# Optimization experiments

Measured on AMD Instinct MI355X. Metric: run time of the kernel, lower is better.

## Reference

```python
import jax, jax.numpy as jnp
import numpy as np

D = 32      # d_shape (internal width, also propagate_dimensions and out_channels)
S = 3       # space_dimensions
K = 40      # kNN neighbors
EPS = 1e-5  # BatchNorm1d eps


def _elu(x):
    return jax.nn.elu(x)


def _batchnorm(x, gamma, beta):
    # training-mode BatchNorm1d over all nodes (flattened batch*nodes), biased var
    mu = x.mean(axis=(0, 1))
    var = x.var(axis=(0, 1))
    return gamma * (x - mu) / jnp.sqrt(var + EPS) + beta


def _knn_mean_max(s, h):
    # s: [N, S] learned coords, h: [N, D] propagated features (one graph)
    N = s.shape[0]
    n2 = jnp.sum(s * s, axis=-1)                     # [N]
    d2 = n2[:, None] + n2[None, :] - 2.0 * (s @ s.T)  # [N, N] squared dists
    d2 = jnp.maximum(d2, 0.0)
    d2 = jnp.where(jnp.eye(N, dtype=bool), jnp.inf, d2)  # exclude self loops
    _, idx = jax.lax.top_k(-d2, K)                   # idx: [N, K] neighbor (src) ids per dst
    d2_sel = jnp.take_along_axis(d2, idx, axis=1)    # [N, K]
    pot = jnp.exp(-d2_sel)                           # gaussian potential exp(-||ds||^2)
    msg = pot[..., None] * h[idx]                    # [N, K, D] edge messages
    return jnp.concatenate([msg.mean(axis=1), msg.max(axis=1)], axis=-1)  # [N, 2D]


def setup_inputs() -> dict:
    key = jax.random.key(0)
    ks = jax.random.split(key, 12)
    B, N, C = 2, 8192, 9

    def lin_w(k, i, o):
        return (jax.random.normal(k, (i, o), jnp.float32) / np.sqrt(i)).astype(jnp.float32)

    return {
        "x": jax.random.normal(ks[0], (B, N, C), jnp.float32),
        # pre_gravnet: Linear(C->32), ELU, Linear(32->32), ELU
        "pre_W1": lin_w(ks[1], C, D), "pre_b1": jnp.zeros((D,), jnp.float32),
        "pre_W2": lin_w(ks[2], D, D), "pre_b2": jnp.zeros((D,), jnp.float32),
        "bn1_g": jnp.ones((D,), jnp.float32), "bn1_b": jnp.zeros((D,), jnp.float32),
        # GravNetConv: lin_s (no bias), lin_h, lin (in = D + 2D -> D)
        "lin_s_W": lin_w(ks[3], D, S),
        "lin_h_W": lin_w(ks[4], D, D), "lin_h_b": jnp.zeros((D,), jnp.float32),
        "lin_W": lin_w(ks[5], D + 2 * D, D), "lin_b": jnp.zeros((D,), jnp.float32),
        # post_gravnet: Linear(D+S+D -> 32), ELU, Linear(32->32), ELU
        "post_W1": lin_w(ks[6], D + S + D, D), "post_b1": jnp.zeros((D,), jnp.float32),
        "post_W2": lin_w(ks[7], D, D), "post_b2": jnp.zeros((D,), jnp.float32),
        "bn2_g": jnp.ones((D,), jnp.float32), "bn2_b": jnp.zeros((D,), jnp.float32),
    }


def reference(x, pre_W1, pre_b1, pre_W2, pre_b2, bn1_g, bn1_b,
              lin_s_W, lin_h_W, lin_h_b, lin_W, lin_b,
              post_W1, post_b1, post_W2, post_b2, bn2_g, bn2_b):
    # pre_gravnet MLP + batchnorm
    x1 = _elu(_elu(x @ pre_W1 + pre_b1) @ pre_W2 + pre_b2)
    x1 = _batchnorm(x1, bn1_g, bn1_b)

    # GravNetConv
    h_l = x1 @ lin_h_W + lin_h_b     # [B, N, D]
    s_l = x1 @ lin_s_W               # [B, N, S] learned coords
    agg = jax.vmap(_knn_mean_max)(s_l, h_l)           # [B, N, 2D]
    xgn = jnp.concatenate([agg, x1], axis=-1) @ lin_W + lin_b  # [B, N, D]

    # post_gravnet MLP + batchnorm
    xc = jnp.concatenate([xgn, s_l, x1], axis=-1)     # [B, N, D+S+D]
    out = _elu(_elu(xc @ post_W1 + post_b1) @ post_W2 + post_b2)
    out = _batchnorm(out, bn2_g, bn2_b)
    return out
```

## Files before the change

### kernel.cpp

```cpp
#include <hip/hip_runtime.h>
#include <math.h>

#define NN    8192
#define NODES 16384
#define KK    40
#define CAP   256


__device__ __forceinline__ float r15_elu(float x){ return x > 0.f ? x : expm1f(x); }

__device__ __forceinline__ unsigned r15_key(float4 si, float4 sj){
  float dot = si.x*sj.x + si.y*sj.y + si.z*sj.z;
  float d2 = si.w + sj.w - 2.0f*dot;
  d2 = fmaxf(d2, 0.0f);
  return __float_as_uint(d2);
}

__global__ __launch_bounds__(256) void r15_pre(const float* __restrict__ x,
    const float* __restrict__ W1, const float* __restrict__ b1,
    const float* __restrict__ W2, const float* __restrict__ b2,
    float* __restrict__ xpre, float* __restrict__ part1)
{
  __shared__ float sW1[9*32], sb1[32], sW2[32*32], sb2[32];
  __shared__ float wls[4][32], wls2[4][32];
  int t = threadIdx.x;
  for (int i = t; i < 9*32;  i += 256) sW1[i] = W1[i];
  for (int i = t; i < 32*32; i += 256) sW2[i] = W2[i];
  if (t < 32) { sb1[t] = b1[t]; sb2[t] = b2[t]; }
  __syncthreads();
  int node = blockIdx.x*256 + t;
  float xv[9], a1[32], a2[32];
  #pragma unroll
  for (int i=0;i<9;i++) xv[i] = x[node*9+i];
  #pragma unroll
  for (int o=0;o<32;o++){
    float a = sb1[o];
    #pragma unroll
    for (int i=0;i<9;i++) a += xv[i]*sW1[i*32+o];
    a1[o] = r15_elu(a);
  }
  #pragma unroll
  for (int o=0;o<32;o++){
    float a = sb2[o];
    #pragma unroll
    for (int i=0;i<32;i++) a += a1[i]*sW2[i*32+o];
    a2[o] = r15_elu(a);
    xpre[(size_t)node*32+o] = a2[o];
  }
  int lane = t & 63, w = t >> 6;
  #pragma unroll
  for (int c=0;c<32;c++){
    float v = a2[c], v2 = a2[c]*a2[c];
    #pragma unroll
    for (int off=32; off; off>>=1){ v += __shfl_down(v,(unsigned)off,64); v2 += __shfl_down(v2,(unsigned)off,64); }
    if (lane==0){ wls[w][c]=v; wls2[w][c]=v2; }
  }
  __syncthreads();
  if (t < 32){
    part1[blockIdx.x*64 + t]      = wls[0][t]+wls[1][t]+wls[2][t]+wls[3][t];
    part1[blockIdx.x*64 + 32 + t] = wls2[0][t]+wls2[1][t]+wls2[2][t]+wls2[3][t];
  }
}

__global__ __launch_bounds__(256) void r15_bnproj(const float* __restrict__ part1,
    const float* __restrict__ xpre,
    const float* __restrict__ bng, const float* __restrict__ bnb,
    const float* __restrict__ hW, const float* __restrict__ hb, const float* __restrict__ sW,
    float* __restrict__ x1, float* __restrict__ h, float4* __restrict__ s4)
{
  __shared__ float sHW[32*32], sHB[32], sSW[32*3];
  __shared__ float sstat[64];
  __shared__ float smu[32], sdev[32], sg[32], sbt[32];
  int t = threadIdx.x;
  for (int i=t;i<1024;i+=256) sHW[i]=hW[i];
  if (t < 96) sSW[t]=sW[t];
  if (t < 64){
    float s = 0.f;
    for (int b2=0;b2<64;b2++) s += part1[b2*64+t];
    sstat[t] = s;
  }
  __syncthreads();
  if (t < 32){
    sHB[t]=hb[t];
    float s = sstat[t], sq = sstat[32+t];
    float mu = s * (1.f/NODES);
    float var = sq * (1.f/NODES) - mu*mu;
    smu[t]=mu; sdev[t]=sqrtf(var+1e-5f);
    sg[t]=bng[t]; sbt[t]=bnb[t];
  }
  __syncthreads();
  int node = blockIdx.x*256+t;
  float v[32];
  #pragma unroll
  for (int c=0;c<32;c++){
    float a = xpre[(size_t)node*32+c];
    v[c] = sg[c]*(a - smu[c])/sdev[c] + sbt[c];
    x1[(size_t)node*32+c] = v[c];
  }
  #pragma unroll
  for (int o=0;o<32;o++){
    float a = sHB[o];
    #pragma unroll
    for (int i=0;i<32;i++) a += v[i]*sHW[i*32+o];
    h[(size_t)node*32+o] = a;
  }
  float s0=0.f,s1=0.f,s2=0.f;
  #pragma unroll
  for (int i=0;i<32;i++){
    s0 += v[i]*sSW[i*3+0];
    s1 += v[i]*sSW[i*3+1];
    s2 += v[i]*sSW[i*3+2];
  }
  float n2 = s0*s0 + s1*s1 + s2*s2;
  s4[node] = make_float4(s0,s1,s2,n2);
}

__global__ __launch_bounds__(256) void r15_knn(const float4* __restrict__ s4,
    const float* __restrict__ h, float* __restrict__ agg)
{
  __shared__ unsigned hist[4][1024];
  __shared__ int      sel[4][KK];
  __shared__ unsigned selk[4][KK];
  __shared__ float    pots[4][KK];
  __shared__ unsigned wsum[4];
  __shared__ unsigned wtot[4][4];
  __shared__ unsigned sB1[4], sL1[4], candCount[4];

  int t = threadIdx.x;
  int lane = t & 63, w = t >> 6;
  int b  = blockIdx.x >> 11;
  int i0 = (blockIdx.x & 2047) * 4;
  const float4* sb = s4 + (size_t)b*NN;
  float4 si[4]; int iq[4];
  #pragma unroll
  for (int q=0;q<4;q++){ iq[q] = i0+q; si[q] = sb[i0+q]; }

  unsigned* histf = (unsigned*)hist;
  #pragma unroll
  for (int z=0; z<16; ++z) histf[z*256 + t] = 0u;
  if (t < 4) candCount[t] = 0u;
  __syncthreads();

  #pragma unroll 2
  for (int c=0;c<32;c++){
    int j = c*256 + t;
    float4 sj = sb[j];
    #pragma unroll
    for (int q=0;q<4;q++){
      unsigned k = r15_key(si[q], sj);
      if (j == iq[q]) k = 0x7F800000u;
      atomicAdd(&hist[q][k>>21], 1u);
    }
  }
  __syncthreads();

  for (int q=0;q<4;q++){
    unsigned c0 = hist[q][4*t+0], c1 = hist[q][4*t+1], c2 = hist[q][4*t+2], c3 = hist[q][4*t+3];
    unsigned chunk = c0+c1+c2+c3;
    unsigned sc = chunk;
    #pragma unroll
    for (int off=1; off<64; off<<=1){
      unsigned o = __shfl_up(sc, (unsigned)off, 64);
      if (lane >= off) sc += o;
    }
    if (lane == 63) wsum[w] = sc;
    __syncthreads();
    unsigned base = 0;
    for (int w2=0; w2<w; ++w2) base += wsum[w2];
    unsigned excl = base + sc - chunk;
    if (excl < KK && KK <= excl + chunk){
      unsigned acc = excl; int bb = 4*t;
      if (acc + c0 >= KK){ sB1[q] = (unsigned)bb;   sL1[q] = acc; }
      else { acc += c0;
        if (acc + c1 >= KK){ sB1[q] = (unsigned)(bb+1); sL1[q] = acc; }
        else { acc += c1;
          if (acc + c2 >= KK){ sB1[q] = (unsigned)(bb+2); sL1[q] = acc; }
          else { acc += c2;    sB1[q] = (unsigned)(bb+3); sL1[q] = acc; } } }
    }
    __syncthreads();
  }
  unsigned B1r[4];
  #pragma unroll
  for (int q=0;q<4;q++) B1r[q] = sB1[q];
  unsigned* candk = &histf[0];
  unsigned* candj = &histf[1024];

  unsigned lessm[4] = {0,0,0,0};
  unsigned cnt[4]   = {0,0,0,0};
  #pragma unroll 2
  for (int c=0;c<32;c++){
    int j = c*256 + t;
    float4 sj = sb[j];
    #pragma unroll
    for (int q=0;q<4;q++){
      unsigned k = r15_key(si[q], sj);
      if (j == iq[q]) k = 0x7F800000u;
      unsigned bin = k >> 21;
      if (bin < B1r[q]){ lessm[q] |= 1u<<c; cnt[q]++; }
      else if (bin == B1r[q]){
        unsigned slot = atomicAdd(&candCount[q], 1u);
        if (slot < CAP){ candk[q*CAP+slot] = k; candj[q*CAP+slot] = (unsigned)j; }
      }
    }
  }
  unsigned vq[4];
  #pragma unroll
  for (int q=0;q<4;q++){
    unsigned v = cnt[q];
    #pragma unroll
    for (int off=1; off<64; off<<=1){
      unsigned o = __shfl_up(v, (unsigned)off, 64);
      if (lane >= off) v += o;
    }
    if (lane == 63) wtot[q][w] = v;
    vq[q] = v;
  }
  __syncthreads();
  #pragma unroll
  for (int q=0;q<4;q++){
    unsigned gbase = 0;
    for (int w2=0; w2<w; ++w2) gbase += wtot[q][w2];
    unsigned offs = gbase + vq[q] - cnt[q];
    unsigned m = lessm[q];
    while (m){
      int c = __builtin_ctz(m); m &= m-1u;
      sel[q][offs++] = c*256 + t;
    }
  }
  __syncthreads();

  for (int q=0;q<4;q++){
    unsigned C1 = candCount[q]; if (C1 > CAP) C1 = CAP;
    unsigned L1 = sL1[q];
    for (unsigned idx = (unsigned)t; idx < C1; idx += 256){
      unsigned k = candk[q*CAP+idx], j = candj[q*CAP+idx];
      unsigned rank = L1;
      for (unsigned u=0; u<C1; ++u){
        unsigned ku = candk[q*CAP+u], ju = candj[q*CAP+u];
        rank += (ku < k || (ku == k && ju < j)) ? 1u : 0u;
      }
      if (rank < KK){ sel[q][rank] = (int)j; selk[q][rank] = k; }
    }
  }
  __syncthreads();
  #pragma unroll
  for (int q=0;q<4;q++){
    if (t < (int)sL1[q]) selk[q][t] = r15_key(si[q], sb[sel[q][t]]);
  }
  __syncthreads();
  if (t < KK){
    #pragma unroll
    for (int q=0;q<4;q++) pots[q][t] = expf(-__uint_as_float(selk[q][t]));
  }
  __syncthreads();

  float (*psum)[32] = (float(*)[32])&histf[2048];
  float (*pmax)[32] = (float(*)[32])&histf[2304];
  int ch = t & 31, g = t >> 5;
  const float* hb2 = h + (size_t)b*NN*32;
  for (int q=0;q<4;q++){
    float sum = 0.f, mx = -INFINITY;
    #pragma unroll
    for (int p=0;p<5;p++){
      int k2 = g*5 + p;
      float m = pots[q][k2] * hb2[(size_t)sel[q][k2]*32 + ch];
      sum += m; mx = fmaxf(mx, m);
    }
    psum[g][ch] = sum; pmax[g][ch] = mx;
    __syncthreads();
    if (t < 32){
      float s = 0.f, m2 = -INFINITY;
      #pragma unroll
      for (int g2=0;g2<8;g2++){ s += psum[g2][t]; m2 = fmaxf(m2, pmax[g2][t]); }
      float* ab = agg + (size_t)(b*NN + i0 + q)*64;
      ab[t]    = s / 40.0f;
      ab[32+t] = m2;
    }
    __syncthreads();
  }
}

__global__ __launch_bounds__(256) void r15_post(const float* __restrict__ agg,
    const float* __restrict__ x1, const float4* __restrict__ s4,
    const float* __restrict__ linW, const float* __restrict__ linb,
    const float* __restrict__ pW1, const float* __restrict__ pb1,
    const float* __restrict__ pW2, const float* __restrict__ pb2,
    float* __restrict__ outpre, float* __restrict__ part2)
{
  __shared__ float sLW[96*32], sPW1[67*32], sPW2[32*32];
  __shared__ float sLB[32], sPB1[32], sPB2[32];
  __shared__ float wls[4][32], wls2[4][32];
  int t = threadIdx.x;
  for (int i=t;i<96*32;i+=256) sLW[i]=linW[i];
  for (int i=t;i<67*32;i+=256) sPW1[i]=pW1[i];
  for (int i=t;i<32*32;i+=256) sPW2[i]=pW2[i];
  if (t<32){ sLB[t]=linb[t]; sPB1[t]=pb1[t]; sPB2[t]=pb2[t]; }
  __syncthreads();
  int node = blockIdx.x*256+t;
  float av[64], xv[32];
  #pragma unroll
  for (int i=0;i<64;i++) av[i]=agg[(size_t)node*64+i];
  #pragma unroll
  for (int i=0;i<32;i++) xv[i]=x1[(size_t)node*32+i];
  float4 sv = s4[node];
  float xgn[32];
  #pragma unroll
  for (int o=0;o<32;o++){
    float a = sLB[o];
    #pragma unroll
    for (int i=0;i<64;i++) a += av[i]*sLW[i*32+o];
    #pragma unroll
    for (int i=0;i<32;i++) a += xv[i]*sLW[(64+i)*32+o];
    xgn[o]=a;
  }
  float p1[32];
  #pragma unroll
  for (int o=0;o<32;o++){
    float a = sPB1[o];
    #pragma unroll
    for (int i=0;i<32;i++) a += xgn[i]*sPW1[i*32+o];
    a += sv.x*sPW1[32*32+o] + sv.y*sPW1[33*32+o] + sv.z*sPW1[34*32+o];
    #pragma unroll
    for (int i=0;i<32;i++) a += xv[i]*sPW1[(35+i)*32+o];
    p1[o]=r15_elu(a);
  }
  float p2[32];
  #pragma unroll
  for (int o=0;o<32;o++){
    float a = sPB2[o];
    #pragma unroll
    for (int i=0;i<32;i++) a += p1[i]*sPW2[i*32+o];
    p2[o] = r15_elu(a);
    outpre[(size_t)node*32+o] = p2[o];
  }
  int lane = t & 63, w = t >> 6;
  #pragma unroll
  for (int c=0;c<32;c++){
    float v = p2[c], v2 = p2[c]*p2[c];
    #pragma unroll
    for (int off=32; off; off>>=1){ v += __shfl_down(v,(unsigned)off,64); v2 += __shfl_down(v2,(unsigned)off,64); }
    if (lane==0){ wls[w][c]=v; wls2[w][c]=v2; }
  }
  __syncthreads();
  if (t < 32){
    part2[blockIdx.x*64 + t]      = wls[0][t]+wls[1][t]+wls[2][t]+wls[3][t];
    part2[blockIdx.x*64 + 32 + t] = wls2[0][t]+wls2[1][t]+wls2[2][t]+wls2[3][t];
  }
}

__global__ __launch_bounds__(256) void r15_bnout(const float* __restrict__ part2,
    const float* __restrict__ outpre,
    const float* __restrict__ g, const float* __restrict__ b,
    float* __restrict__ out)
{
  __shared__ float sstat[64];
  __shared__ float smu[32], sdev2[32], sg2[32], sb2[32];
  int t = threadIdx.x;
  if (t < 64){
    float s = 0.f;
    for (int b2=0;b2<64;b2++) s += part2[b2*64+t];
    sstat[t] = s;
  }
  __syncthreads();
  if (t < 32){
    float s = sstat[t], sq = sstat[32+t];
    float mu = s * (1.f/NODES);
    float var = sq*(1.f/NODES) - mu*mu;
    smu[t] = mu; sdev2[t] = sqrtf(var+1e-5f);
    sg2[t] = g[t]; sb2[t] = b[t];
  }
  __syncthreads();
  int idx = blockIdx.x*256 + t;
  int c = idx & 31;
  out[idx] = sg2[c]*(outpre[idx]-smu[c])/sdev2[c] + sb2[c];
}

extern "C" void kernel_launch(void* const* d_in, const int* in_sizes, int n_in,
                              void* d_out, int out_size, void* d_ws, size_t ws_size,
                              hipStream_t stream)
{
  (void)in_sizes; (void)n_in; (void)out_size; (void)ws_size;
  const float* x      = (const float*)d_in[0];
  const float* preW1  = (const float*)d_in[1];
  const float* preb1  = (const float*)d_in[2];
  const float* preW2  = (const float*)d_in[3];
  const float* preb2  = (const float*)d_in[4];
  const float* bn1g   = (const float*)d_in[5];
  const float* bn1b   = (const float*)d_in[6];
  const float* linsW  = (const float*)d_in[7];
  const float* linhW  = (const float*)d_in[8];
  const float* linhb  = (const float*)d_in[9];
  const float* linW   = (const float*)d_in[10];
  const float* linb   = (const float*)d_in[11];
  const float* postW1 = (const float*)d_in[12];
  const float* postb1 = (const float*)d_in[13];
  const float* postW2 = (const float*)d_in[14];
  const float* postb2 = (const float*)d_in[15];
  const float* bn2g   = (const float*)d_in[16];
  const float* bn2b   = (const float*)d_in[17];

  float* ws = (float*)d_ws;
  float* xpre   = ws;
  float* x1     = xpre   + (size_t)NODES*32;
  float* h      = x1     + (size_t)NODES*32;
  float* s4     = h      + (size_t)NODES*32;
  float* agg    = s4     + (size_t)NODES*4;
  float* outpre = agg    + (size_t)NODES*64;
  float* part1  = outpre + (size_t)NODES*32;
  float* part2  = part1  + 64*64;

  hipLaunchKernelGGL(r15_pre,    dim3(64),    dim3(256), 0, stream, x, preW1, preb1, preW2, preb2, xpre, part1);
  hipLaunchKernelGGL(r15_bnproj, dim3(64),    dim3(256), 0, stream, part1, xpre, bn1g, bn1b, linhW, linhb, linsW, x1, h, (float4*)s4);
  hipLaunchKernelGGL(r15_knn,    dim3(4096),  dim3(256), 0, stream, (const float4*)s4, h, agg);
  hipLaunchKernelGGL(r15_post,   dim3(64),    dim3(256), 0, stream, agg, x1, (const float4*)s4, linW, linb, postW1, postb1, postW2, postb2, outpre, part2);
  hipLaunchKernelGGL(r15_bnout,  dim3(2048),  dim3(256), 0, stream, part2, outpre, bn2g, bn2b, (float*)d_out);
}
```

Before: 233.4 us.

## Pack kNN histograms into 16-bit halves and process queries per-wave in parallel

The kNN kernel packs two queries' histograms into the low and high 16-bit halves of each shared word, halving histogram LDS from 16KB to 8KB. The threshold-bin search now runs one query per wavefront in parallel with no block-level barriers, where before it looped over queries with two syncs each. Candidate ranking and the mean/max reduction are likewise split per wave or per query, with a single barrier. This is meant to cut barrier count and LDS footprint, which may raise occupancy. The 16-bit counters are safe since each query has at most 8192 neighbours.

Measured after the change: 229.1 us. No clear change (-1.8%).

```diff
diff --git a/kernel.cpp b/kernel.cpp
--- a/kernel.cpp
+++ b/kernel.cpp
@@ -7,16 +7,16 @@
 #define CAP   256
 
 
-__device__ __forceinline__ float r15_elu(float x){ return x > 0.f ? x : expm1f(x); }
-
-__device__ __forceinline__ unsigned r15_key(float4 si, float4 sj){
+__device__ __forceinline__ float r16_elu(float x){ return x > 0.f ? x : expm1f(x); }
+
+__device__ __forceinline__ unsigned r16_key(float4 si, float4 sj){
   float dot = si.x*sj.x + si.y*sj.y + si.z*sj.z;
   float d2 = si.w + sj.w - 2.0f*dot;
   d2 = fmaxf(d2, 0.0f);
   return __float_as_uint(d2);
 }
 
-__global__ __launch_bounds__(256) void r15_pre(const float* __restrict__ x,
+__global__ __launch_bounds__(256) void r16_pre(const float* __restrict__ x,
     const float* __restrict__ W1, const float* __restrict__ b1,
     const float* __restrict__ W2, const float* __restrict__ b2,
     float* __restrict__ xpre, float* __restrict__ part1)
@@ -37,14 +37,14 @@
     float a = sb1[o];
     #pragma unroll
     for (int i=0;i<9;i++) a += xv[i]*sW1[i*32+o];
-    a1[o] = r15_elu(a);
+    a1[o] = r16_elu(a);
   }
   #pragma unroll
   for (int o=0;o<32;o++){
     float a = sb2[o];
     #pragma unroll
     for (int i=0;i<32;i++) a += a1[i]*sW2[i*32+o];
-    a2[o] = r15_elu(a);
+    a2[o] = r16_elu(a);
     xpre[(size_t)node*32+o] = a2[o];
   }
   int lane = t & 63, w = t >> 6;
@@ -62,7 +62,7 @@
   }
 }
 
-__global__ __launch_bounds__(256) void r15_bnproj(const float* __restrict__ part1,
+__global__ __launch_bounds__(256) void r16_bnproj(const float* __restrict__ part1,
     const float* __restrict__ xpre,
     const float* __restrict__ bng, const float* __restrict__ bnb,
     const float* __restrict__ hW, const float* __restrict__ hb, const float* __restrict__ sW,
@@ -115,14 +115,13 @@
   s4[node] = make_float4(s0,s1,s2,n2);
 }
 
-__global__ __launch_bounds__(256) void r15_knn(const float4* __restrict__ s4,
+__global__ __launch_bounds__(256) void r16_knn(const float4* __restrict__ s4,
     const float* __restrict__ h, float* __restrict__ agg)
 {
-  __shared__ unsigned hist[4][1024];
+  __shared__ unsigned hist[2][1024];
   __shared__ int      sel[4][KK];
   __shared__ unsigned selk[4][KK];
   __shared__ float    pots[4][KK];
-  __shared__ unsigned wsum[4];
   __shared__ unsigned wtot[4][4];
   __shared__ unsigned sB1[4], sL1[4], candCount[4];
 
@@ -137,7 +136,7 @@
 
   unsigned* histf = (unsigned*)hist;
   #pragma unroll
-  for (int z=0; z<16; ++z) histf[z*256 + t] = 0u;
+  for (int z=0; z<8; ++z) histf[z*256 + t] = 0u;
   if (t < 4) candCount[t] = 0u;
   __syncthreads();
 
@@ -147,38 +146,40 @@
     float4 sj = sb[j];
     #pragma unroll
     for (int q=0;q<4;q++){
-      unsigned k = r15_key(si[q], sj);
+      unsigned k = r16_key(si[q], sj);
       if (j == iq[q]) k = 0x7F800000u;
-      atomicAdd(&hist[q][k>>21], 1u);
-    }
-  }
-  __syncthreads();
-
-  for (int q=0;q<4;q++){
-    unsigned c0 = hist[q][4*t+0], c1 = hist[q][4*t+1], c2 = hist[q][4*t+2], c3 = hist[q][4*t+3];
-    unsigned chunk = c0+c1+c2+c3;
+      atomicAdd(&hist[q&1][k>>21], (q>>1) ? 0x10000u : 1u);
+    }
+  }
+  __syncthreads();
+
+  {
+    int q = w;
+    unsigned c16[16]; unsigned chunk = 0;
+    int base = lane*16;
+    #pragma unroll
+    for (int jj=0;jj<16;jj++){
+      unsigned word = hist[q&1][base+jj];
+      unsigned cc = (q>>1) ? (word >> 16) : (word & 0xFFFFu);
+      c16[jj] = cc; chunk += cc;
+    }
     unsigned sc = chunk;
     #pragma unroll
     for (int off=1; off<64; off<<=1){
       unsigned o = __shfl_up(sc, (unsigned)off, 64);
       if (lane >= off) sc += o;
     }
-    if (lane == 63) wsum[w] = sc;
-    __syncthreads();
-    unsigned base = 0;
-    for (int w2=0; w2<w; ++w2) base += wsum[w2];
-    unsigned excl = base + sc - chunk;
-    if (excl < KK && KK <= excl + chunk){
-      unsigned acc = excl; int bb = 4*t;
-      if (acc + c0 >= KK){ sB1[q] = (unsigned)bb;   sL1[q] = acc; }
-      else { acc += c0;
-        if (acc + c1 >= KK){ sB1[q] = (unsigned)(bb+1); sL1[q] = acc; }
-        else { acc += c1;
-          if (acc + c2 >= KK){ sB1[q] = (unsigned)(bb+2); sL1[q] = acc; }
-          else { acc += c2;    sB1[q] = (unsigned)(bb+3); sL1[q] = acc; } } }
-    }
-    __syncthreads();
-  }
+    unsigned excl = sc - chunk;
+    if (excl < KK && KK <= sc){
+      unsigned acc = excl;
+      #pragma unroll
+      for (int jj=0;jj<16;jj++){
+        if (acc + c16[jj] >= KK){ sB1[q] = (unsigned)(base+jj); sL1[q] = acc; break; }
+        acc += c16[jj];
+      }
+    }
+  }
+  __syncthreads();
   unsigned B1r[4];
   #pragma unroll
   for (int q=0;q<4;q++) B1r[q] = sB1[q];
@@ -193,7 +194,7 @@
     float4 sj = sb[j];
     #pragma unroll
     for (int q=0;q<4;q++){
-      unsigned k = r15_key(si[q], sj);
+      unsigned k = r16_key(si[q], sj);
       if (j == iq[q]) k = 0x7F800000u;
       unsigned bin = k >> 21;
       if (bin < B1r[q]){ lessm[q] |= 1u<<c; cnt[q]++; }
@@ -229,10 +230,11 @@
   }
   __syncthreads();
 
-  for (int q=0;q<4;q++){
+  {
+    int q = t >> 6;
     unsigned C1 = candCount[q]; if (C1 > CAP) C1 = CAP;
     unsigned L1 = sL1[q];
-    for (unsigned idx = (unsigned)t; idx < C1; idx += 256){
+    for (unsigned idx = (unsigned)lane; idx < C1; idx += 64){
       unsigned k = candk[q*CAP+idx], j = candj[q*CAP+idx];
       unsigned rank = L1;
       for (unsigned u=0; u<C1; ++u){
@@ -245,7 +247,7 @@
   __syncthreads();
   #pragma unroll
   for (int q=0;q<4;q++){
-    if (t < (int)sL1[q]) selk[q][t] = r15_key(si[q], sb[sel[q][t]]);
+    if (t < (int)sL1[q]) selk[q][t] = r16_key(si[q], sb[sel[q][t]]);
   }
   __syncthreads();
   if (t < KK){
@@ -254,10 +256,11 @@
   }
   __syncthreads();
 
-  float (*psum)[32] = (float(*)[32])&histf[2048];
-  float (*pmax)[32] = (float(*)[32])&histf[2304];
+  float (*psum)[8][32] = (float(*)[8][32])&histf[0];
+  float (*pmax)[8][32] = (float(*)[8][32])&histf[1024];
   int ch = t & 31, g = t >> 5;
   const float* hb2 = h + (size_t)b*NN*32;
+  #pragma unroll
   for (int q=0;q<4;q++){
     float sum = 0.f, mx = -INFINITY;
     #pragma unroll
@@ -266,21 +269,21 @@
       float m = pots[q][k2] * hb2[(size_t)sel[q][k2]*32 + ch];
       sum += m; mx = fmaxf(mx, m);
     }
-    psum[g][ch] = sum; pmax[g][ch] = mx;
-    __syncthreads();
-    if (t < 32){
-      float s = 0.f, m2 = -INFINITY;
-      #pragma unroll
-      for (int g2=0;g2<8;g2++){ s += psum[g2][t]; m2 = fmaxf(m2, pmax[g2][t]); }
-      float* ab = agg + (size_t)(b*NN + i0 + q)*64;
-      ab[t]    = s / 40.0f;
-      ab[32+t] = m2;
-    }
-    __syncthreads();
-  }
-}
-
-__global__ __launch_bounds__(256) void r15_post(const float* __restrict__ agg,
+    psum[q][g][ch] = sum; pmax[q][g][ch] = mx;
+  }
+  __syncthreads();
+  if (t < 128){
+    int q = t >> 5, c2 = t & 31;
+    float s = 0.f, m2 = -INFINITY;
+    #pragma unroll
+    for (int g2=0;g2<8;g2++){ s += psum[q][g2][c2]; m2 = fmaxf(m2, pmax[q][g2][c2]); }
+    float* ab = agg + (size_t)(b*NN + i0 + q)*64;
+    ab[c2]    = s / 40.0f;
+    ab[32+c2] = m2;
+  }
+}
+
+__global__ __launch_bounds__(256) void r16_post(const float* __restrict__ agg,
     const float* __restrict__ x1, const float4* __restrict__ s4,
     const float* __restrict__ linW, const float* __restrict__ linb,
     const float* __restrict__ pW1, const float* __restrict__ pb1,
@@ -322,7 +325,7 @@
     a += sv.x*sPW1[32*32+o] + sv.y*sPW1[33*32+o] + sv.z*sPW1[34*32+o];
     #pragma unroll
     for (int i=0;i<32;i++) a += xv[i]*sPW1[(35+i)*32+o];
-    p1[o]=r15_elu(a);
+    p1[o]=r16_elu(a);
   }
   float p2[32];
   #pragma unroll
@@ -330,7 +333,7 @@
     float a = sPB2[o];
     #pragma unroll
     for (int i=0;i<32;i++) a += p1[i]*sPW2[i*32+o];
-    p2[o] = r15_elu(a);
+    p2[o] = r16_elu(a);
     outpre[(size_t)node*32+o] = p2[o];
   }
   int lane = t & 63, w = t >> 6;
@@ -348,7 +351,7 @@
   }
 }
 
-__global__ __launch_bounds__(256) void r15_bnout(const float* __restrict__ part2,
+__global__ __launch_bounds__(256) void r16_bnout(const float* __restrict__ part2,
     const float* __restrict__ outpre,
     const float* __restrict__ g, const float* __restrict__ b,
     float* __restrict__ out)
@@ -409,9 +412,9 @@
   float* part1  = outpre + (size_t)NODES*32;
   float* part2  = part1  + 64*64;
 
-  hipLaunchKernelGGL(r15_pre,    dim3(64),    dim3(256), 0, stream, x, preW1, preb1, preW2, preb2, xpre, part1);
-  hipLaunchKernelGGL(r15_bnproj, dim3(64),    dim3(256), 0, stream, part1, xpre, bn1g, bn1b, linhW, linhb, linsW, x1, h, (float4*)s4);
-  hipLaunchKernelGGL(r15_knn,    dim3(4096),  dim3(256), 0, stream, (const float4*)s4, h, agg);
-  hipLaunchKernelGGL(r15_post,   dim3(64),    dim3(256), 0, stream, agg, x1, (const float4*)s4, linW, linb, postW1, postb1, postW2, postb2, outpre, part2);
-  hipLaunchKernelGGL(r15_bnout,  dim3(2048),  dim3(256), 0, stream, part2, outpre, bn2g, bn2b, (float*)d_out);
-}
+  hipLaunchKernelGGL(r16_pre,    dim3(64),    dim3(256), 0, stream, x, preW1, preb1, preW2, preb2, xpre, part1);
+  hipLaunchKernelGGL(r16_bnproj, dim3(64),    dim3(256), 0, stream, part1, xpre, bn1g, bn1b, linhW, linhb, linsW, x1, h, (float4*)s4);
+  hipLaunchKernelGGL(r16_knn,    dim3(4096),  dim3(256), 0, stream, (const float4*)s4, h, agg);
+  hipLaunchKernelGGL(r16_post,   dim3(64),    dim3(256), 0, stream, agg, x1, (const float4*)s4, linW, linb, postW1, postb1, postW2, postb2, outpre, part2);
+  hipLaunchKernelGGL(r16_bnout,  dim3(2048),  dim3(256), 0, stream, part2, outpre, bn2g, bn2b, (float*)d_out);
+}
```
